# Kernel tuning notes

Hardware: AMD Instinct MI355X
Metric: run time of the kernel (lower is better)

## Reference

```python
import jax, jax.numpy as jnp
import numpy as np

MARGIN = 1.0


def setup_inputs() -> dict:
    key = jax.random.key(0)
    k1, k2 = jax.random.split(key)
    inputs = jax.random.normal(k1, (512, 256), dtype=jnp.float32)
    targets = jax.random.randint(k2, (512,), 0, 64)
    return {"inputs": inputs, "targets": targets}


def reference(inputs, targets):
    n = inputs.shape[0]
    # pairwise euclidean distance matrix [n, n]
    sq = jnp.sum(inputs * inputs, axis=1)
    dist = sq[:, None] + sq[None, :] - 2.0 * (inputs @ inputs.T)
    dist = jnp.sqrt(jnp.clip(dist, 1e-16))

    # triplet margins: ap_dist[i,j] - an_dist[i,k] + margin -> [n, n, n]
    triplet = dist[:, :, None] - dist[:, None, :] + MARGIN

    # mask: i != j, i != k, j != k, labels[i]==labels[j], labels[i]!=labels[k]
    not_eye = ~jnp.eye(n, dtype=bool)
    dist_idx = not_eye[:, :, None] & not_eye[:, None, :] & not_eye[None, :, :]
    teq = targets[:, None] == targets[None, :]  # symmetric [n, n]
    valid = teq[:, :, None] & (~teq[:, None, :])
    mask = (valid & dist_idx).astype(triplet.dtype)

    triplet = jnp.maximum(mask * triplet, 0.0)
    num_triplets = jnp.sum((triplet > 1e-16).astype(triplet.dtype))
    return jnp.sum(triplet) / (num_triplets + 1e-16)
```

## Files before the change

### kernel.cpp

```cpp
#include <hip/hip_runtime.h>

constexpr int N = 512;
constexpr int D = 256;
#define MARGIN 1.0f

#define ACC(S, A, B)                                                   \
  { float ex = A.x - B.x, ey = A.y - B.y, ez = A.z - B.z,              \
          ew = A.w - B.w;                                              \
    S += ex * ex + ey * ey + ez * ez + ew * ew; }

__global__ __launch_bounds__(1024, 4) void triplet_fused(
    const float* __restrict__ x, const int* __restrict__ tgt,
    float* __restrict__ part) {
  __shared__ __align__(16) float m0[N], m1[N];
  __shared__ float cl0[N], cl1[N];
  __shared__ int nv0, nv1;
  __shared__ float wred[32];

  const int b = blockIdx.x;
  const int i0 = 2 * b, i1 = 2 * b + 1;
  const int tid = threadIdx.x;
  const int wave = tid >> 6, lane = tid & 63;
  const int sub = lane & 15, rg = lane >> 4;
  const int t0 = tgt[i0], t1 = tgt[i1];

  if (tid == 0) { nv0 = 0; nv1 = 0; }

  const float4* xa = (const float4*)(x + (size_t)i0 * D);
  const float4* xc = (const float4*)(x + (size_t)i1 * D);
  float4 a0 = xa[sub], a1 = xa[16 + sub], a2 = xa[32 + sub], a3 = xa[48 + sub];
  float4 c0 = xc[sub], c1 = xc[16 + sub], c2 = xc[32 + sub], c3 = xc[48 + sub];
  __syncthreads();

  const int rot = (b * 171) & (N - 1);
  const int rbase = wave * 32 + rg;
  #pragma unroll 2
  for (int it = 0; it < 8; ++it) {
    const int r = (rbase + it * 4 + rot) & (N - 1);
    const float4* xr = (const float4*)(x + (size_t)r * D);
    float4 b0 = xr[sub];
    float4 b1 = xr[16 + sub];
    float4 b2 = xr[32 + sub];
    float4 b3 = xr[48 + sub];
    float sa = 0.f, sb = 0.f;
    ACC(sa, a0, b0); ACC(sa, a1, b1); ACC(sa, a2, b2); ACC(sa, a3, b3);
    ACC(sb, c0, b0); ACC(sb, c1, b1); ACC(sb, c2, b2); ACC(sb, c3, b3);
    #pragma unroll
    for (int off = 8; off > 0; off >>= 1) {
      sa += __shfl_down(sa, off);
      sb += __shfl_down(sb, off);
    }
    if (sub == 0) {
      const int tj = tgt[r];
      float da = sqrtf(fmaxf(sa, 1e-16f));
      float db = sqrtf(fmaxf(sb, 1e-16f));
      m0[r] = (tj != t0) ? da : __builtin_inff();
      m1[r] = (tj != t1) ? db : __builtin_inff();
      if (tj == t0 && r != i0) { int s = atomicAdd(&nv0, 1); cl0[s] = da + MARGIN; }
      if (tj == t1 && r != i1) { int s = atomicAdd(&nv1, 1); cl1[s] = db + MARGIN; }
    }
  }
  __syncthreads();

  float sum = 0.f, cnt = 0.f;
  const int e = tid & 511, half = tid >> 9;
  const float mk0 = m0[e], mk1 = m1[e];
  const int n0 = nv0, n1 = nv1;
  for (int v = half; v < n0; v += 2) {
    float a = cl0[v] - mk0;
    sum += fmaxf(a, 0.f);
    cnt += (a > 1e-16f ? 1.f : 0.f);
  }
  for (int v = half; v < n1; v += 2) {
    float a = cl1[v] - mk1;
    sum += fmaxf(a, 0.f);
    cnt += (a > 1e-16f ? 1.f : 0.f);
  }

  #pragma unroll
  for (int off = 32; off > 0; off >>= 1) {
    sum += __shfl_down(sum, off);
    cnt += __shfl_down(cnt, off);
  }
  if (lane == 0) { wred[wave] = sum; wred[16 + wave] = cnt; }
  __syncthreads();
  if (tid == 0) {
    float s = 0.f, c = 0.f;
    #pragma unroll
    for (int w = 0; w < 16; ++w) { s += wred[w]; c += wred[16 + w]; }
    part[2 * b] = s;
    part[2 * b + 1] = c;
  }
}

__global__ __launch_bounds__(256) void triplet_finalize(
    const float* __restrict__ part, float* __restrict__ out) {
  __shared__ float wred[8];
  const int tid = threadIdx.x;
  float s = part[2 * tid], c = part[2 * tid + 1];
  #pragma unroll
  for (int off = 32; off > 0; off >>= 1) {
    s += __shfl_down(s, off);
    c += __shfl_down(c, off);
  }
  int wave = tid >> 6, lane = tid & 63;
  if (lane == 0) { wred[wave] = s; wred[4 + wave] = c; }
  __syncthreads();
  if (tid == 0) {
    float ts = wred[0] + wred[1] + wred[2] + wred[3];
    float tc = wred[4] + wred[5] + wred[6] + wred[7];
    out[0] = ts / (tc + 1e-16f);
  }
}

extern "C" void kernel_launch(void* const* d_in, const int* in_sizes, int n_in,
                              void* d_out, int out_size, void* d_ws, size_t ws_size,
                              hipStream_t stream) {
  const float* x = (const float*)d_in[0];
  const int* tgt = (const int*)d_in[1];
  float* out = (float*)d_out;
  float* part = (float*)d_ws;

  triplet_fused<<<N / 2, 1024, 0, stream>>>(x, tgt, part);
  triplet_finalize<<<1, 256, 0, stream>>>(part, out);
}
```

Measured before the change: 66.49 us.

## Fuse finalize into main kernel via flag-based last-stage reduction in block 0

Removes the separate finalize launch: each block publishes its partial sum and count with a release-stored flag tagged by block index, and block 0 spin-waits on all flags before reducing and writing the output. Targets are also staged into shared memory so the per-row label reads come from LDS instead of global memory. This saves a kernel launch and its gap, but block 0 busy-waits and relies on every block being resident or eventually scheduled. The tagged flag values are not cleared between calls, so a stale flag from an earlier call could be read as current.

```diff
diff --git a/kernel.cpp b/kernel.cpp
--- a/kernel.cpp
+++ b/kernel.cpp
@@ -2,7 +2,9 @@
 
 constexpr int N = 512;
 constexpr int D = 256;
+constexpr int NB = 256;
 #define MARGIN 1.0f
+
 
 #define ACC(S, A, B)                                                   \
   { float ex = A.x - B.x, ey = A.y - B.y, ez = A.z - B.z,              \
@@ -11,9 +13,11 @@
 
 __global__ __launch_bounds__(1024, 4) void triplet_fused(
     const float* __restrict__ x, const int* __restrict__ tgt,
-    float* __restrict__ part) {
+    float* __restrict__ part, int* __restrict__ flags,
+    float* __restrict__ out) {
   __shared__ __align__(16) float m0[N], m1[N];
   __shared__ float cl0[N], cl1[N];
+  __shared__ int stgt[N];
   __shared__ int nv0, nv1;
   __shared__ float wred[32];
 
@@ -22,15 +26,16 @@
   const int tid = threadIdx.x;
   const int wave = tid >> 6, lane = tid & 63;
   const int sub = lane & 15, rg = lane >> 4;
-  const int t0 = tgt[i0], t1 = tgt[i1];
 
   if (tid == 0) { nv0 = 0; nv1 = 0; }
+  if (tid < N / 2) ((int2*)stgt)[tid] = ((const int2*)tgt)[tid];
 
   const float4* xa = (const float4*)(x + (size_t)i0 * D);
   const float4* xc = (const float4*)(x + (size_t)i1 * D);
   float4 a0 = xa[sub], a1 = xa[16 + sub], a2 = xa[32 + sub], a3 = xa[48 + sub];
   float4 c0 = xc[sub], c1 = xc[16 + sub], c2 = xc[32 + sub], c3 = xc[48 + sub];
   __syncthreads();
+  const int t0 = stgt[i0], t1 = stgt[i1];
 
   const int rot = (b * 171) & (N - 1);
   const int rbase = wave * 32 + rg;
@@ -51,7 +56,7 @@
       sb += __shfl_down(sb, off);
     }
     if (sub == 0) {
-      const int tj = tgt[r];
+      const int tj = stgt[r];
       float da = sqrtf(fmaxf(sa, 1e-16f));
       float db = sqrtf(fmaxf(sb, 1e-16f));
       m0[r] = (tj != t0) ? da : __builtin_inff();
@@ -88,28 +93,40 @@
     float s = 0.f, c = 0.f;
     #pragma unroll
     for (int w = 0; w < 16; ++w) { s += wred[w]; c += wred[16 + w]; }
-    part[2 * b] = s;
-    part[2 * b + 1] = c;
+    __hip_atomic_store(&part[2 * b], s, __ATOMIC_RELAXED, __HIP_MEMORY_SCOPE_AGENT);
+    __hip_atomic_store(&part[2 * b + 1], c, __ATOMIC_RELAXED, __HIP_MEMORY_SCOPE_AGENT);
+    __hip_atomic_store(&flags[b], (int)(0xC0FFEE00 | b), __ATOMIC_RELEASE,
+                       __HIP_MEMORY_SCOPE_AGENT);
   }
-}
 
-__global__ __launch_bounds__(256) void triplet_finalize(
-    const float* __restrict__ part, float* __restrict__ out) {
-  __shared__ float wred[8];
-  const int tid = threadIdx.x;
-  float s = part[2 * tid], c = part[2 * tid + 1];
-  #pragma unroll
-  for (int off = 32; off > 0; off >>= 1) {
-    s += __shfl_down(s, off);
-    c += __shfl_down(c, off);
-  }
-  int wave = tid >> 6, lane = tid & 63;
-  if (lane == 0) { wred[wave] = s; wred[4 + wave] = c; }
-  __syncthreads();
-  if (tid == 0) {
-    float ts = wred[0] + wred[1] + wred[2] + wred[3];
-    float tc = wred[4] + wred[5] + wred[6] + wred[7];
-    out[0] = ts / (tc + 1e-16f);
+  if (b == 0) {
+    if (tid < NB) {
+      const int expect = (int)(0xC0FFEE00 | tid);
+      while (__hip_atomic_load(&flags[tid], __ATOMIC_ACQUIRE,
+                               __HIP_MEMORY_SCOPE_AGENT) != expect) {
+        __builtin_amdgcn_s_sleep(4);
+      }
+    }
+    __syncthreads();
+    float s = 0.f, c = 0.f;
+    if (tid < NB) {
+      s = __hip_atomic_load(&part[2 * tid], __ATOMIC_RELAXED,
+                            __HIP_MEMORY_SCOPE_AGENT);
+      c = __hip_atomic_load(&part[2 * tid + 1], __ATOMIC_RELAXED,
+                            __HIP_MEMORY_SCOPE_AGENT);
+    }
+    #pragma unroll
+    for (int off = 32; off > 0; off >>= 1) {
+      s += __shfl_down(s, off);
+      c += __shfl_down(c, off);
+    }
+    if (lane == 0 && tid < NB) { wred[wave] = s; wred[16 + wave] = c; }
+    __syncthreads();
+    if (tid == 0) {
+      float ts = wred[0] + wred[1] + wred[2] + wred[3];
+      float tc = wred[16] + wred[17] + wred[18] + wred[19];
+      out[0] = ts / (tc + 1e-16f);
+    }
   }
 }
 
@@ -120,7 +137,7 @@
   const int* tgt = (const int*)d_in[1];
   float* out = (float*)d_out;
   float* part = (float*)d_ws;
+  int* flags = (int*)((float*)d_ws + 2 * NB);
 
-  triplet_fused<<<N / 2, 1024, 0, stream>>>(x, tgt, part);
-  triplet_finalize<<<1, 256, 0, stream>>>(part, out);
+  triplet_fused<<<NB, 1024, 0, stream>>>(x, tgt, part, flags, out);
 }
```

Result: no change. 67.45 us (+1.4%).
